# Kernel optimization log

Hardware: AMD Instinct MI355X
Metric: run time of the kernel (lower is better)

The kernel has to match this reference:

```python
import jax, jax.numpy as jnp
import numpy as np

D_MODEL = 2048
N_HEADS = 32
N_KV = 8
HEAD_DIM = D_MODEL // N_HEADS  # 64
ROPE_BASE = 500000.0


def _rope_tables(seq_len, dim, dtype):
    inv_freq = 1.0 / (ROPE_BASE ** (jnp.arange(0, dim, 2, dtype=jnp.float32) / dim))
    t = jnp.arange(seq_len, dtype=jnp.float32)
    freqs = jnp.outer(t, inv_freq)          # [S, dim/2]
    emb = jnp.concatenate([freqs, freqs], axis=-1)  # [S, dim]
    return jnp.cos(emb).astype(dtype), jnp.sin(emb).astype(dtype)


def _rotate_half(x):
    x1, x2 = jnp.split(x, 2, axis=-1)
    return jnp.concatenate([-x2, x1], axis=-1)


def setup_inputs() -> dict:
    key = jax.random.key(0)
    ks = jax.random.split(key, 5)
    B, S = 2, 2048
    sc = 0.02
    return {
        "x": jax.random.normal(ks[0], (B, S, D_MODEL), jnp.float32),
        "Wq": jax.random.normal(ks[1], (D_MODEL, N_HEADS * HEAD_DIM), jnp.float32) * sc,
        "Wk": jax.random.normal(ks[2], (D_MODEL, N_KV * HEAD_DIM), jnp.float32) * sc,
        "Wv": jax.random.normal(ks[3], (D_MODEL, N_KV * HEAD_DIM), jnp.float32) * sc,
        "Wo": jax.random.normal(ks[4], (N_HEADS * HEAD_DIM, D_MODEL), jnp.float32) * sc,
    }


def reference(x, Wq, Wk, Wv, Wo):
    B, S, _ = x.shape
    n_rep = N_HEADS // N_KV

    q = (x @ Wq).reshape(B, S, N_HEADS, HEAD_DIM)
    k = (x @ Wk).reshape(B, S, N_KV, HEAD_DIM)
    v = (x @ Wv).reshape(B, S, N_KV, HEAD_DIM)

    cos, sin = _rope_tables(S, HEAD_DIM, x.dtype)
    cos = cos[None, :, None, :]  # [1,S,1,D]
    sin = sin[None, :, None, :]
    q = q * cos + _rotate_half(q) * sin
    k = k * cos + _rotate_half(k) * sin

    # GQA without materializing expanded K/V: group q heads by kv head.
    qg = q.reshape(B, S, N_KV, n_rep, HEAD_DIM)
    scale = 1.0 / jnp.sqrt(jnp.asarray(HEAD_DIM, x.dtype))
    # scores: [B, n_kv, n_rep, Sq, Sk]
    scores = jnp.einsum("bqhrd,bkhd->bhrqk", qg, k) * scale
    attn = jax.nn.softmax(scores, axis=-1)
    out = jnp.einsum("bhrqk,bkhd->bqhrd", attn, v)  # [B,S,n_kv,n_rep,D]
    out = out.reshape(B, S, N_HEADS * HEAD_DIM)
    return out @ Wo
```

## Files before the change

### kernel.cpp

```cpp
#include <hip/hip_runtime.h>
#include <hip/hip_bf16.h>
#include <stdint.h>

#define SS    2048
#define BB    2
#define MT    4096
#define DM    2048
#define NQKVC 3072

typedef __attribute__((ext_vector_type(8))) short s16x8;
typedef __attribute__((ext_vector_type(4))) short s16x4;
typedef __attribute__((ext_vector_type(4))) float f32x4;
typedef __attribute__((ext_vector_type(2))) unsigned u32x2;

typedef __attribute__((address_space(1))) const void* as1cv;
typedef __attribute__((address_space(3))) void* as3v;

__device__ __forceinline__ float b2f(int u) {
  union { unsigned u; float f; } x; x.u = ((unsigned)(u & 0xFFFF)) << 16; return x.f;
}
__device__ __forceinline__ short f2b(float f) {
  union { float f; unsigned u; } x; x.f = f;
  unsigned r = x.u + 0x7FFFu + ((x.u >> 16) & 1u);
  return (short)(r >> 16);
}
__device__ __forceinline__ void gld16(const void* g, void* l) {
  __builtin_amdgcn_global_load_lds((as1cv)(uintptr_t)g, (as3v)(uint32_t)(uintptr_t)l, 16, 0, 0);
}
__device__ __forceinline__ s16x8 ldsfrag(const char* tile, int r, int cb) {
  return *(const s16x8*)(tile + r * 128 + (cb ^ ((r & 7) << 4)));
}
__device__ __forceinline__ f32x4 mfma16(s16x8 a, s16x8 b, f32x4 c) {
  return __builtin_amdgcn_mfma_f32_16x16x32_bf16(a, b, c, 0, 0, 0);
}
__device__ __forceinline__ void swz8(int& bx, int& by) {
  int gx = gridDim.x;
  int lin = by * gx + bx;
  int tot = gx * gridDim.y;
  int s = (lin & 7) * (tot >> 3) + (lin >> 3);
  bx = s % gx;
  by = s / gx;
}

__global__ __launch_bounds__(256) void k_wpre(const float* __restrict__ x,
                                              const float* __restrict__ Wq,
                                              const float* __restrict__ Wk,
                                              const float* __restrict__ Wv,
                                              const float* __restrict__ Wo,
                                              ushort* __restrict__ xb,
                                              ushort* __restrict__ Wqkvt,
                                              ushort* __restrict__ Wot,
                                              float* __restrict__ rtab) {
  __shared__ float t[32][33];
  int bid = blockIdx.x;
  if (bid < 8192) {
    int i = (bid * 256 + threadIdx.x) * 4;
    float4 v = *(const float4*)(x + i);
    s16x4 o = { f2b(v.x), f2b(v.y), f2b(v.z), f2b(v.w) };
    *(s16x4*)(xb + i) = o;
    return;
  }
  bid -= 8192;
  if (bid >= 10240) {
    int idx = (bid - 10240) * 256 + threadIdx.x;
    int d = idx & 31, s = idx >> 5;
    float invf = exp2f(-(float)d * (18.931568569324174f / 32.0f));
    float sn, c;
    sincosf((float)s * invf, &sn, &c);
    rtab[idx * 2]     = c;
    rtab[idx * 2 + 1] = sn;
    return;
  }
  const float* W; ushort* out; int N; int l;
  if (bid < 4096)      { W = Wq; out = Wqkvt;                         N = 2048; l = bid; }
  else if (bid < 5120) { W = Wk; out = Wqkvt + (size_t)2048 * 2048;   N = 512;  l = bid - 4096; }
  else if (bid < 6144) { W = Wv; out = Wqkvt + (size_t)2560 * 2048;   N = 512;  l = bid - 5120; }
  else                 { W = Wo; out = Wot;                           N = 2048; l = bid - 6144; }
  int k0 = (l & 63) * 32, n0 = (l >> 6) * 32;
  int tx = threadIdx.x & 31, ty = threadIdx.x >> 5;
#pragma unroll
  for (int j = 0; j < 32; j += 8)
    t[ty + j][tx] = W[(size_t)(k0 + ty + j) * N + n0 + tx];
  __syncthreads();
#pragma unroll
  for (int j = 0; j < 32; j += 8)
    out[(size_t)(n0 + ty + j) * 2048 + k0 + tx] = (ushort)f2b(t[tx][ty + j]);
}

__global__ __launch_bounds__(256) void k_vt(const ushort* __restrict__ QKV,
                                            ushort* __restrict__ Vt) {
  __shared__ ushort t[32][33];
  int s0 = blockIdx.x * 32;
  int c0 = (blockIdx.y & 15) * 32;
  int b  = blockIdx.y >> 4;
  int tx = threadIdx.x & 31, ty = threadIdx.x >> 5;
#pragma unroll
  for (int j = 0; j < 32; j += 8)
    t[ty + j][tx] = QKV[(size_t)(b * SS + s0 + ty + j) * NQKVC + 2560 + c0 + tx];
  __syncthreads();
#pragma unroll
  for (int j = 0; j < 32; j += 8)
    Vt[(size_t)(b * 512 + c0 + ty + j) * SS + s0 + tx] = t[tx][ty + j];
}

template <int BF16_OUT, int ROPE>
__global__ __launch_bounds__(256) void k_gemm(const ushort* __restrict__ A,
                                              const ushort* __restrict__ B,
                                              void* __restrict__ Cv,
                                              const float* __restrict__ rtab,
                                              int M, int N, int K) {
  __shared__ __align__(16) char lds[32768];
  char* ldsA = lds;
  char* ldsB = lds + 16384;
  int bx = blockIdx.x, by = blockIdx.y;
  swz8(bx, by);
  int tid = threadIdx.x, lane = tid & 63, wid = tid >> 6;
  int wr = wid >> 1, wc = wid & 1;
  int row0 = by * 128, col0 = bx * 128;
  int fr = lane & 15, fq = lane >> 4;
  f32x4 acc[4][4] = {};
  int rl = lane >> 3;
  int cbs = ((lane & 7) << 4) ^ (rl << 4);
  const char* Ab = (const char*)A;
  const char* Bb = (const char*)B;
  size_t ldb = (size_t)K * 2;

  for (int kt = 0; kt < K; kt += 64) {
#pragma unroll
    for (int i = 0; i < 4; i++) {
      int ra = wid * 32 + i * 8 + rl;
      gld16(Ab + (size_t)(row0 + ra) * ldb + (size_t)kt * 2 + cbs,
            ldsA + (wid * 32 + i * 8) * 128);
      gld16(Bb + (size_t)(col0 + ra) * ldb + (size_t)kt * 2 + cbs,
            ldsB + (wid * 32 + i * 8) * 128);
    }
    __syncthreads();
#pragma unroll
    for (int kk = 0; kk < 2; kk++) {
      int cb = kk * 64 + (fq << 4);
      s16x8 af[4], bg[4];
#pragma unroll
      for (int m = 0; m < 4; m++) af[m] = ldsfrag(ldsA, wr * 64 + m * 16 + fr, cb);
#pragma unroll
      for (int n = 0; n < 4; n++) bg[n] = ldsfrag(ldsB, wc * 64 + n * 16 + fr, cb);
#pragma unroll
      for (int m = 0; m < 4; m++)
#pragma unroll
        for (int n = 0; n < 4; n++)
          acc[m][n] = mfma16(af[m], bg[n], acc[m][n]);
    }
    __syncthreads();
  }

  if (ROPE) {
    int cb0 = col0 + wc * 64;
    if (cb0 < 2560) {
      float qs = (cb0 < 2048) ? 0.18033688011112042f : 1.0f;
#pragma unroll
      for (int m = 0; m < 4; m++)
#pragma unroll
        for (int i = 0; i < 4; i++) {
          int srow = (row0 + wr * 64 + m * 16 + fq * 4 + i) & (SS - 1);
          const float* tr = rtab + srow * 64;
          float cs0 = tr[fr * 2],        sn0 = tr[fr * 2 + 1];
          float cs1 = tr[32 + fr * 2],   sn1 = tr[32 + fr * 2 + 1];
          float lo0 = acc[m][0][i], hi0 = acc[m][2][i];
          acc[m][0][i] = (lo0 * cs0 - hi0 * sn0) * qs;
          acc[m][2][i] = (hi0 * cs0 + lo0 * sn0) * qs;
          float lo1 = acc[m][1][i], hi1 = acc[m][3][i];
          acc[m][1][i] = (lo1 * cs1 - hi1 * sn1) * qs;
          acc[m][3][i] = (hi1 * cs1 + lo1 * sn1) * qs;
        }
    }
  }

#pragma unroll
  for (int m = 0; m < 4; m++) {
#pragma unroll
    for (int i = 0; i < 4; i++) {
      int row = row0 + wr * 64 + m * 16 + fq * 4 + i;
      if (BF16_OUT) {
        ushort* C = (ushort*)Cv;
#pragma unroll
        for (int n = 0; n < 4; n++)
          C[(size_t)row * N + col0 + wc * 64 + n * 16 + fr] = (ushort)f2b(acc[m][n][i]);
      } else {
        float* C = (float*)Cv;
#pragma unroll
        for (int n = 0; n < 4; n++)
          C[(size_t)row * N + col0 + wc * 64 + n * 16 + fr] = acc[m][n][i];
      }
    }
  }
}

__global__ __launch_bounds__(256) void k_attn(const ushort* __restrict__ QKV,
                                              const ushort* __restrict__ Vt,
                                              ushort* __restrict__ O) {
  __shared__ __align__(16) char ldsK[16384];
  __shared__ __align__(16) char ldsV[16384];
  __shared__ __align__(16) char ldsP[4][2048];
  int bx = blockIdx.x, by = blockIdx.y;
  swz8(bx, by);
  int tid = threadIdx.x, lane = tid & 63, wid = tid >> 6;
  int bh = by, b = bh >> 5, h = bh & 31, kv = h >> 2;
  int fr = lane & 15, fq = lane >> 4;
  int q0 = bx * 128 + wid * 32;

  s16x8 qf[2][2];
#pragma unroll
  for (int kk = 0; kk < 2; kk++)
#pragma unroll
    for (int qi = 0; qi < 2; qi++)
      qf[kk][qi] = *(const s16x8*)(QKV + (size_t)(b * SS + q0 + qi * 16 + fr) * NQKVC
                                   + h * 64 + kk * 32 + fq * 8);

  const f32x4 fz = {0.f, 0.f, 0.f, 0.f};
  f32x4 o[4][2];
  f32x4 psum[2] = {fz, fz};
#pragma unroll
  for (int n = 0; n < 4; n++) { o[n][0] = fz; o[n][1] = fz; }
  const short ONE = 0x3F80;
  const s16x8 ones = {ONE, ONE, ONE, ONE, ONE, ONE, ONE, ONE};

  int rl = lane >> 3;
  int cbs = ((lane & 7) << 4) ^ (rl << 4);
  const char* Kbase = (const char*)QKV + (size_t)(b * SS) * (NQKVC * 2) + (size_t)(2048 + kv * 64) * 2;
  const char* Vbase = (const char*)Vt + (size_t)((b * 8 + kv) * 64) * (SS * 2);
  char* pw = ldsP[wid];
  int pswz = (fr & 7) << 4;

  for (int t = 0; t < SS / 128; t++) {
#pragma unroll
    for (int j = 0; j < 4; j++) {
      int rr = wid * 32 + j * 8;
      gld16(Kbase + (size_t)(t * 128 + rr + rl) * (NQKVC * 2) + cbs, ldsK + rr * 128);
    }
#pragma unroll
    for (int hh = 0; hh < 2; hh++)
#pragma unroll
      for (int j = 0; j < 2; j++) {
        int rr = wid * 16 + j * 8;
        gld16(Vbase + (size_t)(rr + rl) * (SS * 2) + (size_t)t * 256 + hh * 128 + cbs,
              ldsV + (hh * 64 + rr) * 128);
      }
    __syncthreads();

#pragma unroll
    for (int hh = 0; hh < 2; hh++) {
      const char* Kc = ldsK + hh * 8192;
      const char* Vc = ldsV + hh * 8192;

      f32x4 sf[4][2];
#pragma unroll
      for (int n = 0; n < 4; n++) { sf[n][0] = fz; sf[n][1] = fz; }
#pragma unroll
      for (int kk = 0; kk < 2; kk++) {
        int cb = kk * 64 + (fq << 4);
#pragma unroll
        for (int n = 0; n < 4; n++) {
          s16x8 kf = ldsfrag(Kc, n * 16 + fr, cb);
          sf[n][0] = mfma16(kf, qf[kk][0], sf[n][0]);
          sf[n][1] = mfma16(kf, qf[kk][1], sf[n][1]);
        }
      }

#pragma unroll
      for (int qi = 0; qi < 2; qi++) {
        char* pwr = pw + fr * 128;
#pragma unroll
        for (int n = 0; n < 4; n++) {
          float e0 = __builtin_amdgcn_exp2f(sf[n][qi][0]);
          float e1 = __builtin_amdgcn_exp2f(sf[n][qi][1]);
          float e2 = __builtin_amdgcn_exp2f(sf[n][qi][2]);
          float e3 = __builtin_amdgcn_exp2f(sf[n][qi][3]);
          unsigned u01, u23;
          asm("v_cvt_pk_bf16_f32 %0, %1, %2" : "=v"(u01) : "v"(e0), "v"(e1));
          asm("v_cvt_pk_bf16_f32 %0, %1, %2" : "=v"(u23) : "v"(e2), "v"(e3));
          u32x2 w = {u01, u23};
          *(u32x2*)(pwr + ((n * 32 + fq * 8) ^ pswz)) = w;
        }
        asm volatile("" ::: "memory");
#pragma unroll
        for (int kk = 0; kk < 2; kk++) {
          int cb = kk * 64 + (fq << 4);
          s16x8 pa = ldsfrag(pw, fr, cb);
          psum[qi] = mfma16(pa, ones, psum[qi]);
#pragma unroll
          for (int n = 0; n < 4; n++) {
            s16x8 vf = ldsfrag(Vc, n * 16 + fr, cb);
            o[n][qi] = mfma16(pa, vf, o[n][qi]);
          }
        }
        asm volatile("" ::: "memory");
      }
    }
    __syncthreads();
  }

#pragma unroll
  for (int qi = 0; qi < 2; qi++) {
    float inv[4];
#pragma unroll
    for (int i = 0; i < 4; i++) inv[i] = 1.0f / psum[qi][i];
#pragma unroll
    for (int n = 0; n < 4; n++) {
      float e0 = o[n][qi][0] * inv[0], e1 = o[n][qi][1] * inv[1];
      float e2 = o[n][qi][2] * inv[2], e3 = o[n][qi][3] * inv[3];
      unsigned u01, u23;
      asm("v_cvt_pk_bf16_f32 %0, %1, %2" : "=v"(u01) : "v"(e0), "v"(e1));
      asm("v_cvt_pk_bf16_f32 %0, %1, %2" : "=v"(u23) : "v"(e2), "v"(e3));
      int colb = n * 32 + fr * 2;
#pragma unroll
      for (int i = 0; i < 4; i++) {
        int r = fq * 4 + i;
        unsigned v16 = (i == 0) ? (u01 & 0xffffu) : (i == 1) ? (u01 >> 16)
                      : (i == 2) ? (u23 & 0xffffu) : (u23 >> 16);
        *(short*)(pw + r * 128 + (colb ^ ((r & 7) << 4))) = (short)v16;
      }
    }
    asm volatile("" ::: "memory");
    int orow = lane >> 2;
    int cbase = (lane & 3) * 32;
    int swo = (orow & 7) << 4;
    s16x8 ov0 = *(const s16x8*)(pw + orow * 128 + (cbase ^ swo));
    s16x8 ov1 = *(const s16x8*)(pw + orow * 128 + ((cbase + 16) ^ swo));
    ushort* dst = O + (size_t)(b * SS + bx * 128 + wid * 32 + qi * 16 + orow) * DM + h * 64 + (lane & 3) * 16;
    *(s16x8*)(dst)     = ov0;
    *(s16x8*)(dst + 8) = ov1;
    asm volatile("" ::: "memory");
  }
}

extern "C" void kernel_launch(void* const* d_in, const int* in_sizes, int n_in,
                              void* d_out, int out_size, void* d_ws, size_t ws_size,
                              hipStream_t stream) {
  const float* x  = (const float*)d_in[0];
  const float* Wq = (const float*)d_in[1];
  const float* Wk = (const float*)d_in[2];
  const float* Wv = (const float*)d_in[3];
  const float* Wo = (const float*)d_in[4];
  char* ws = (char*)d_ws;
  ushort* xb    = (ushort*)(ws);
  ushort* Wqkvt = (ushort*)(ws + 16777216);
  ushort* Wot   = (ushort*)(ws + 29360128);
  ushort* QKV   = (ushort*)(ws + 37748736);
  ushort* Vt    = (ushort*)(ws + 62914560);
  ushort* Obuf  = (ushort*)(ws + 67108864);
  float* rtab = (ws_size >= (size_t)83886080 + 524288)
              ? (float*)(ws + 83886080) : (float*)d_out;

  k_wpre<<<18688, 256, 0, stream>>>(x, Wq, Wk, Wv, Wo, xb, Wqkvt, Wot, rtab);
  k_gemm<1, 1><<<dim3(24, 32), 256, 0, stream>>>(xb, Wqkvt, (void*)QKV, rtab, MT, NQKVC, DM);
  k_vt<<<dim3(64, 32), 256, 0, stream>>>(QKV, Vt);
  k_attn<<<dim3(16, 64), 256, 0, stream>>>(QKV, Vt, Obuf);
  k_gemm<0, 0><<<dim3(16, 32), 256, 0, stream>>>(Obuf, Wot, d_out, nullptr, MT, DM, DM);
}
```

Before: 241.5 us.

## Fuse V transpose into QKV GEMM epilogue and widen weight-prep stores

Tiles of the QKV GEMM that cover the V columns now transpose their accumulators through LDS and write V directly in transposed layout, skipping the QKV store for V. This removes the separate k_vt kernel launch and its extra global read/write of V. The weight-prep kernel also writes pairs of bf16 values per thread instead of single values. The risks are LDS reuse hazards and a little extra epilogue work in the V tiles.

```diff
diff --git a/kernel.cpp b/kernel.cpp
--- a/kernel.cpp
+++ b/kernel.cpp
@@ -82,25 +82,15 @@
   for (int j = 0; j < 32; j += 8)
     t[ty + j][tx] = W[(size_t)(k0 + ty + j) * N + n0 + tx];
   __syncthreads();
-#pragma unroll
-  for (int j = 0; j < 32; j += 8)
-    out[(size_t)(n0 + ty + j) * 2048 + k0 + tx] = (ushort)f2b(t[tx][ty + j]);
-}
-
-__global__ __launch_bounds__(256) void k_vt(const ushort* __restrict__ QKV,
-                                            ushort* __restrict__ Vt) {
-  __shared__ ushort t[32][33];
-  int s0 = blockIdx.x * 32;
-  int c0 = (blockIdx.y & 15) * 32;
-  int b  = blockIdx.y >> 4;
-  int tx = threadIdx.x & 31, ty = threadIdx.x >> 5;
-#pragma unroll
-  for (int j = 0; j < 32; j += 8)
-    t[ty + j][tx] = QKV[(size_t)(b * SS + s0 + ty + j) * NQKVC + 2560 + c0 + tx];
-  __syncthreads();
-#pragma unroll
-  for (int j = 0; j < 32; j += 8)
-    Vt[(size_t)(b * 512 + c0 + ty + j) * SS + s0 + tx] = t[tx][ty + j];
+  int tx2 = threadIdx.x & 15, rr = threadIdx.x >> 4;
+#pragma unroll
+  for (int j = 0; j < 32; j += 16) {
+    int nl = rr + j;
+    ushort2 w;
+    w.x = (ushort)f2b(t[tx2 * 2][nl]);
+    w.y = (ushort)f2b(t[tx2 * 2 + 1][nl]);
+    *(ushort2*)(out + (size_t)(n0 + nl) * 2048 + k0 + tx2 * 2) = w;
+  }
 }
 
 template <int BF16_OUT, int ROPE>
@@ -108,6 +98,7 @@
                                               const ushort* __restrict__ B,
                                               void* __restrict__ Cv,
                                               const float* __restrict__ rtab,
+                                              ushort* __restrict__ Vt,
                                               int M, int N, int K) {
   __shared__ __align__(16) char lds[32768];
   char* ldsA = lds;
@@ -152,8 +143,37 @@
     __syncthreads();
   }
 
+  int cb0 = col0 + wc * 64;
+
+  if (ROPE && col0 >= 2560) {
+    __syncthreads();
+    char* tw = lds + wid * 8192;
+#pragma unroll
+    for (int m = 0; m < 4; m++)
+#pragma unroll
+      for (int n = 0; n < 4; n++) {
+        int cl = n * 16 + fr;
+        unsigned u01, u23;
+        asm("v_cvt_pk_bf16_f32 %0, %1, %2" : "=v"(u01) : "v"(acc[m][n][0]), "v"(acc[m][n][1]));
+        asm("v_cvt_pk_bf16_f32 %0, %1, %2" : "=v"(u23) : "v"(acc[m][n][2]), "v"(acc[m][n][3]));
+        u32x2 w = {u01, u23};
+        *(u32x2*)(tw + cl * 128 + (((m * 16 + fq * 4) * 2) ^ ((cl & 7) << 4))) = w;
+      }
+    asm volatile("" ::: "memory");
+    int b = row0 >> 11;
+    int s0 = row0 - b * 2048 + wr * 64;
+    int vrow0 = b * 512 + (cb0 - 2560);
+#pragma unroll
+    for (int jj = 0; jj < 8; jj++) {
+      int cl = jj * 8 + (lane >> 3);
+      int ch = lane & 7;
+      s16x8 v = *(const s16x8*)(tw + cl * 128 + ((ch * 16) ^ ((cl & 7) << 4)));
+      *(s16x8*)(Vt + (size_t)(vrow0 + cl) * SS + s0 + ch * 8) = v;
+    }
+    return;
+  }
+
   if (ROPE) {
-    int cb0 = col0 + wc * 64;
     if (cb0 < 2560) {
       float qs = (cb0 < 2048) ? 0.18033688011112042f : 1.0f;
 #pragma unroll
@@ -351,8 +371,7 @@
               ? (float*)(ws + 83886080) : (float*)d_out;
 
   k_wpre<<<18688, 256, 0, stream>>>(x, Wq, Wk, Wv, Wo, xb, Wqkvt, Wot, rtab);
-  k_gemm<1, 1><<<dim3(24, 32), 256, 0, stream>>>(xb, Wqkvt, (void*)QKV, rtab, MT, NQKVC, DM);
-  k_vt<<<dim3(64, 32), 256, 0, stream>>>(QKV, Vt);
+  k_gemm<1, 1><<<dim3(24, 32), 256, 0, stream>>>(xb, Wqkvt, (void*)QKV, rtab, Vt, MT, NQKVC, DM);
   k_attn<<<dim3(16, 64), 256, 0, stream>>>(QKV, Vt, Obuf);
-  k_gemm<0, 0><<<dim3(16, 32), 256, 0, stream>>>(Obuf, Wot, d_out, nullptr, MT, DM, DM);
-}
+  k_gemm<0, 0><<<dim3(16, 32), 256, 0, stream>>>(Obuf, Wot, d_out, nullptr, nullptr, MT, DM, DM);
+}
```

New measurement: 239.0 us, median of 2. About the same (-1.0%).
